# Optimization experiments

Measured on AMD Instinct MI355X. Metric: run time of the kernel, lower is better.

Reference implementation:

```python
import jax, jax.numpy as jnp
import numpy as np

N = 4096      # nodes
F = 128       # input feature dim
HEADS = 8     # attention_num
U = 8         # units per head


def setup_inputs() -> dict:
    key = jax.random.key(0)
    k_a, k_h, k_w, k_al, k_ar = jax.random.split(key, 5)
    A = jax.random.randint(k_a, (N, N), 0, 2).astype(jnp.float32)   # dense 0/1 adjacency
    H = jax.random.normal(k_h, (N, F), dtype=jnp.float32)
    W = jax.random.normal(k_w, (HEADS, F, U), dtype=jnp.float32) * 0.1
    a_left = jax.random.normal(k_al, (HEADS, U), dtype=jnp.float32) * 0.1
    a_right = jax.random.normal(k_ar, (HEADS, U), dtype=jnp.float32) * 0.1
    return {"A": A, "H": H, "W": W, "a_left": a_left, "a_right": a_right}


def reference(A, H, W, a_left, a_right):
    # Per-head attention logits: E[h,i,j] = e_left[h,i] + e_right[h,j]
    e_l = jnp.einsum('nf,hfu,hu->hn', H, W, a_left)    # [HEADS, N]
    e_r = jnp.einsum('nf,hfu,hu->hn', H, W, a_right)   # [HEADS, N]
    E = e_l[:, :, None] + e_r[:, None, :]              # [HEADS, N, N]
    # Faithful to original: denominator uses exp(E * A) (zeros in A -> exp(0)=1)
    denom = jnp.sum(jnp.exp(E * A[None]), axis=-1, keepdims=True)   # [HEADS, N, 1]
    Alpha = jnp.exp(E) / denom * A[None]               # masked attention weights
    # Aggregate then project: elu(Alpha @ H @ W) per head
    out = jax.nn.elu(jnp.einsum('hij,jf,hfu->hiu', Alpha, H, W))    # [HEADS, N, U]
    # is_output_layer=False -> concat heads along feature dim: [N, HEADS*U]
    return jnp.transpose(out, (1, 0, 2)).reshape(H.shape[0], HEADS * U)
```

## Files before the change

### kernel.cpp

```cpp
#include <hip/hip_runtime.h>
#include <hip/hip_bf16.h>

#define NN 4096
#define FF 128
#define NC 80
#define LSTR 84

typedef __attribute__((ext_vector_type(4))) float float4v;
typedef __attribute__((ext_vector_type(4))) unsigned int uint4v;
typedef __attribute__((ext_vector_type(8))) short short8;

static __device__ inline unsigned short bfb(float x) {
    __hip_bfloat16 b = __float2bfloat16(x);
    return *(unsigned short*)&b;
}
static __device__ inline float bff(unsigned short u) {
    __hip_bfloat16 b = *(__hip_bfloat16*)&u;
    return __bfloat162float(b);
}

__global__ __launch_bounds__(256) void gat_wsplit(const float* __restrict__ W,
                                                  const float* __restrict__ al,
                                                  const float* __restrict__ ar,
                                                  __hip_bfloat16* __restrict__ Wphi,
                                                  __hip_bfloat16* __restrict__ Wplo)
{
    const int tid = blockIdx.x * 256 + threadIdx.x;
    if (tid >= 80 * FF) return;
    const int c = tid % 80;
    const int f = tid / 80;
    float val;
    if (c < 64) {
        val = W[(size_t)(c >> 3) * (FF * 8) + (size_t)f * 8 + (c & 7)];
    } else {
        const int hc = (c - 64) & 7;
        const float* ap = (c < 72) ? ar : al;
        const float* wp = W + (size_t)hc * (FF * 8) + (size_t)f * 8;
        float s = 0.f;
        #pragma unroll
        for (int u = 0; u < 8; ++u) s += wp[u] * ap[hc * 8 + u];
        val = s;
    }
    const unsigned short h = bfb(val);
    const unsigned short l = bfb(val - bff(h));
    const int g = (f >> 5) * 4 + ((f >> 3) & 3);
    const size_t idx = ((size_t)g * NC + c) * 8 + (f & 7);
    Wphi[idx] = *(const __hip_bfloat16*)&h;
    Wplo[idx] = *(const __hip_bfloat16*)&l;
}

__global__ __launch_bounds__(64, 1) void gat_prep(const float* __restrict__ H,
                                                  const __hip_bfloat16* __restrict__ Wphi,
                                                  const __hip_bfloat16* __restrict__ Wplo,
                                                  float* __restrict__ expEl,
                                                  __hip_bfloat16* __restrict__ Bp)
{
    const int lane = threadIdx.x;
    const int j0 = blockIdx.x * 16;
    const int m16 = lane & 15, q = lane >> 4;
    const short* Whs = (const short*)Wphi;
    const short* Wls = (const short*)Wplo;

    float4v acc[5] = {};
    #pragma unroll
    for (int kt = 0; kt < 4; ++kt) {
        const float* hp = H + (size_t)(j0 + m16) * FF + kt * 32 + q * 8;
        float4v x0 = *(const float4v*)hp;
        float4v x1 = *(const float4v*)(hp + 4);
        short8 ahi, alo;
        #pragma unroll
        for (int i = 0; i < 4; ++i) {
            const unsigned short h0 = bfb(x0[i]);
            ahi[i] = (short)h0;
            alo[i] = (short)bfb(x0[i] - bff(h0));
            const unsigned short h1 = bfb(x1[i]);
            ahi[4 + i] = (short)h1;
            alo[4 + i] = (short)bfb(x1[i] - bff(h1));
        }
        const short8* bh = (const short8*)(Whs + (size_t)(kt * 4 + q) * NC * 8);
        const short8* bl = (const short8*)(Wls + (size_t)(kt * 4 + q) * NC * 8);
        #pragma unroll
        for (int nt = 0; nt < 5; ++nt) {
            short8 bhi = bh[nt * 16 + m16];
            short8 blo = bl[nt * 16 + m16];
            acc[nt] = __builtin_amdgcn_mfma_f32_16x16x32_bf16(ahi, bhi, acc[nt], 0, 0, 0);
            acc[nt] = __builtin_amdgcn_mfma_f32_16x16x32_bf16(alo, bhi, acc[nt], 0, 0, 0);
            acc[nt] = __builtin_amdgcn_mfma_f32_16x16x32_bf16(ahi, blo, acc[nt], 0, 0, 0);
        }
    }

    const int jbase = j0 + q * 4;
    float ex[4];
    #pragma unroll
    for (int r = 0; r < 4; ++r) ex[r] = expf(acc[4][r]);
    if (m16 >= 8) {
        #pragma unroll
        for (int r = 0; r < 4; ++r)
            expEl[(m16 - 8) * NN + jbase + r] = ex[r];
    }
    #pragma unroll
    for (int r = 0; r < 4; ++r) {
        const int j = jbase + r;
        const size_t base = ((size_t)((j >> 5) * 4 + ((j >> 3) & 3)) * NC) * 8 + (j & 7);
        #pragma unroll
        for (int nt = 0; nt < 4; ++nt) {
            const int srcl = (lane & 48) | (nt * 2 + (m16 >> 3));
            const float er = __shfl(ex[r], srcl);
            Bp[base + (size_t)(nt * 16 + m16) * 8] = __float2bfloat16(er * acc[nt][r]);
        }
        const float v = (m16 < 8) ? ex[r] : (m16 == 8 ? 1.0f : 0.0f);
        Bp[base + (size_t)(64 + m16) * 8] = __float2bfloat16(v);
    }
}

__global__ __launch_bounds__(512) void gat_gemm(const float* __restrict__ A,
                                                const __hip_bfloat16* __restrict__ Bp,
                                                const float* __restrict__ expEl,
                                                float* __restrict__ out)
{
    __shared__ float Ls[8 * 16 * LSTR];
    const int rb   = blockIdx.x;
    const int wave = threadIdx.x >> 6;
    const int lane = threadIdx.x & 63;
    const int m16  = lane & 15;
    const int q    = lane >> 4;
    const int row0 = rb * 16;

    float4v acc[5] = {};

    const int k0 = wave * 512;
    const unsigned int* Au = (const unsigned int*)A;
    const short* Bs = (const short*)Bp;
    const unsigned int* arow = Au + (size_t)(row0 + m16) * NN + q * 8;

    uint4v a0 = *(const uint4v*)(arow + k0);
    uint4v a1 = *(const uint4v*)(arow + k0 + 4);

    #pragma unroll 4
    for (int kt = 0; kt < 16; ++kt) {
        const int kk = k0 + kt * 32;
        short8 afrag;
        afrag[0] = (short)(a0[0] >> 16); afrag[1] = (short)(a0[1] >> 16);
        afrag[2] = (short)(a0[2] >> 16); afrag[3] = (short)(a0[3] >> 16);
        afrag[4] = (short)(a1[0] >> 16); afrag[5] = (short)(a1[1] >> 16);
        afrag[6] = (short)(a1[2] >> 16); afrag[7] = (short)(a1[3] >> 16);

        if (kt + 1 < 16) {
            a0 = *(const uint4v*)(arow + kk + 32);
            a1 = *(const uint4v*)(arow + kk + 36);
        }

        const int ktg = kk >> 5;
        const short8* bbase = (const short8*)(Bs + ((size_t)(ktg * 4 + q) * NC) * 8);
        #pragma unroll
        for (int nt = 0; nt < 5; ++nt) {
            short8 bfrag = bbase[nt * 16 + m16];
            acc[nt] = __builtin_amdgcn_mfma_f32_16x16x32_bf16(afrag, bfrag, acc[nt], 0, 0, 0);
        }
    }

    float* Lw = Ls + wave * (16 * LSTR);
    #pragma unroll
    for (int nt = 0; nt < 5; ++nt) {
        #pragma unroll
        for (int r = 0; r < 4; ++r)
            Lw[(q * 4 + r) * LSTR + nt * 16 + m16] = acc[nt][r];
    }
    __syncthreads();

    #pragma unroll
    for (int p = threadIdx.x; p < 1024; p += 512) {
        const int il = p >> 6;
        const int c  = p & 63;
        const int h  = c >> 3;
        float T = 0.f, S = 0.f, dg = 0.f;
        #pragma unroll
        for (int w = 0; w < 8; ++w) {
            const float* rowp = Ls + w * (16 * LSTR) + il * LSTR;
            T  += rowp[c];
            S  += rowp[64 + h];
            dg += rowp[72];
        }
        const float el = expEl[h * NN + row0 + il];
        const float denom = ((float)NN - dg) + el * S;
        const float x = el * T / denom;
        out[(size_t)(row0 + il) * 64 + c] = x > 0.f ? x : expf(x) - 1.f;
    }
}

extern "C" void kernel_launch(void* const* d_in, const int* in_sizes, int n_in,
                              void* d_out, int out_size, void* d_ws, size_t ws_size,
                              hipStream_t stream) {
    const float* A  = (const float*)d_in[0];
    const float* H  = (const float*)d_in[1];
    const float* W  = (const float*)d_in[2];
    const float* al = (const float*)d_in[3];
    const float* ar = (const float*)d_in[4];
    float* out = (float*)d_out;

    float* expEl = (float*)d_ws;
    __hip_bfloat16* Bp   = (__hip_bfloat16*)((char*)d_ws + 131072);
    __hip_bfloat16* Wphi = (__hip_bfloat16*)((char*)d_ws + 131072 + 655360);
    __hip_bfloat16* Wplo = (__hip_bfloat16*)((char*)d_ws + 131072 + 655360 + 20480);

    gat_wsplit<<<40, 256, 0, stream>>>(W, al, ar, Wphi, Wplo);
    gat_prep<<<NN / 16, 64, 0, stream>>>(H, Wphi, Wplo, expEl, Bp);
    gat_gemm<<<NN / 16, 512, 0, stream>>>(A, Bp, expEl, out);
}
```

Before: 119.8 us.

## Split prep K-loop across four waves and double-buffer A loads in GEMM

The prep kernel now runs four waves per block. Each wave handles one 32-wide K slice, the partial products are reduced through shared memory, and the exp/scaling and Bp/expEl writes are redistributed across 256 threads. This adds parallelism to a kernel that previously used a single wave per block. The GEMM kernel prefetches the A tiles two iterations ahead with a fully unrolled loop, to hide global load latency better. The cost is extra LDS traffic and a block barrier in prep, plus more registers in the GEMM.

```diff
diff --git a/kernel.cpp b/kernel.cpp
--- a/kernel.cpp
+++ b/kernel.cpp
@@ -49,67 +49,84 @@
     Wplo[idx] = *(const __hip_bfloat16*)&l;
 }
 
-__global__ __launch_bounds__(64, 1) void gat_prep(const float* __restrict__ H,
-                                                  const __hip_bfloat16* __restrict__ Wphi,
-                                                  const __hip_bfloat16* __restrict__ Wplo,
-                                                  float* __restrict__ expEl,
-                                                  __hip_bfloat16* __restrict__ Bp)
+__global__ __launch_bounds__(256) void gat_prep(const float* __restrict__ H,
+                                                const __hip_bfloat16* __restrict__ Wphi,
+                                                const __hip_bfloat16* __restrict__ Wplo,
+                                                float* __restrict__ expEl,
+                                                __hip_bfloat16* __restrict__ Bp)
 {
-    const int lane = threadIdx.x;
-    const int j0 = blockIdx.x * 16;
-    const int m16 = lane & 15, q = lane >> 4;
+    __shared__ float Lp[4 * 16 * LSTR];
+    const int t    = threadIdx.x;
+    const int wave = t >> 6;
+    const int lane = t & 63;
+    const int j0   = blockIdx.x * 16;
+    const int m16  = lane & 15, q = lane >> 4;
     const short* Whs = (const short*)Wphi;
     const short* Wls = (const short*)Wplo;
-
+    const int kt = wave;
+
+    const float* hp = H + (size_t)(j0 + m16) * FF + kt * 32 + q * 8;
+    float4v x0 = *(const float4v*)hp;
+    float4v x1 = *(const float4v*)(hp + 4);
+    short8 ahi, alo;
+    #pragma unroll
+    for (int i = 0; i < 4; ++i) {
+        const unsigned short h0 = bfb(x0[i]);
+        ahi[i] = (short)h0;
+        alo[i] = (short)bfb(x0[i] - bff(h0));
+        const unsigned short h1 = bfb(x1[i]);
+        ahi[4 + i] = (short)h1;
+        alo[4 + i] = (short)bfb(x1[i] - bff(h1));
+    }
+
+    const short8* bh = (const short8*)(Whs + (size_t)(kt * 4 + q) * NC * 8);
+    const short8* bl = (const short8*)(Wls + (size_t)(kt * 4 + q) * NC * 8);
     float4v acc[5] = {};
     #pragma unroll
-    for (int kt = 0; kt < 4; ++kt) {
-        const float* hp = H + (size_t)(j0 + m16) * FF + kt * 32 + q * 8;
-        float4v x0 = *(const float4v*)hp;
-        float4v x1 = *(const float4v*)(hp + 4);
-        short8 ahi, alo;
-        #pragma unroll
-        for (int i = 0; i < 4; ++i) {
-            const unsigned short h0 = bfb(x0[i]);
-            ahi[i] = (short)h0;
-            alo[i] = (short)bfb(x0[i] - bff(h0));
-            const unsigned short h1 = bfb(x1[i]);
-            ahi[4 + i] = (short)h1;
-            alo[4 + i] = (short)bfb(x1[i] - bff(h1));
-        }
-        const short8* bh = (const short8*)(Whs + (size_t)(kt * 4 + q) * NC * 8);
-        const short8* bl = (const short8*)(Wls + (size_t)(kt * 4 + q) * NC * 8);
-        #pragma unroll
-        for (int nt = 0; nt < 5; ++nt) {
-            short8 bhi = bh[nt * 16 + m16];
-            short8 blo = bl[nt * 16 + m16];
-            acc[nt] = __builtin_amdgcn_mfma_f32_16x16x32_bf16(ahi, bhi, acc[nt], 0, 0, 0);
-            acc[nt] = __builtin_amdgcn_mfma_f32_16x16x32_bf16(alo, bhi, acc[nt], 0, 0, 0);
-            acc[nt] = __builtin_amdgcn_mfma_f32_16x16x32_bf16(ahi, blo, acc[nt], 0, 0, 0);
-        }
-    }
-
-    const int jbase = j0 + q * 4;
-    float ex[4];
-    #pragma unroll
-    for (int r = 0; r < 4; ++r) ex[r] = expf(acc[4][r]);
-    if (m16 >= 8) {
+    for (int nt = 0; nt < 5; ++nt) {
+        short8 bhi = bh[nt * 16 + m16];
+        short8 blo = bl[nt * 16 + m16];
+        acc[nt] = __builtin_amdgcn_mfma_f32_16x16x32_bf16(ahi, bhi, acc[nt], 0, 0, 0);
+        acc[nt] = __builtin_amdgcn_mfma_f32_16x16x32_bf16(alo, bhi, acc[nt], 0, 0, 0);
+        acc[nt] = __builtin_amdgcn_mfma_f32_16x16x32_bf16(ahi, blo, acc[nt], 0, 0, 0);
+    }
+
+    float* Lw = Lp + wave * (16 * LSTR);
+    #pragma unroll
+    for (int nt = 0; nt < 5; ++nt) {
         #pragma unroll
         for (int r = 0; r < 4; ++r)
-            expEl[(m16 - 8) * NN + jbase + r] = ex[r];
-    }
-    #pragma unroll
-    for (int r = 0; r < 4; ++r) {
-        const int j = jbase + r;
-        const size_t base = ((size_t)((j >> 5) * 4 + ((j >> 3) & 3)) * NC) * 8 + (j & 7);
-        #pragma unroll
-        for (int nt = 0; nt < 4; ++nt) {
-            const int srcl = (lane & 48) | (nt * 2 + (m16 >> 3));
-            const float er = __shfl(ex[r], srcl);
-            Bp[base + (size_t)(nt * 16 + m16) * 8] = __float2bfloat16(er * acc[nt][r]);
-        }
-        const float v = (m16 < 8) ? ex[r] : (m16 == 8 ? 1.0f : 0.0f);
-        Bp[base + (size_t)(64 + m16) * 8] = __float2bfloat16(v);
+            Lw[(q * 4 + r) * LSTR + nt * 16 + m16] = acc[nt][r];
+    }
+    __syncthreads();
+
+    const int jl = t >> 4, g = t & 15;
+    const float* Lr = Lp + jl * LSTR;
+    const int jg = j0 + jl;
+    const size_t base = ((size_t)((jg >> 5) * 4 + ((jg >> 3) & 3)) * NC) * 8 + (jg & 7);
+
+    #pragma unroll
+    for (int i = 0; i < 4; ++i) {
+        const int c = g + 16 * i;
+        const int h = (g >> 3) + 2 * i;
+        const float er = expf(Lr[64 + h] + Lr[16 * LSTR + 64 + h] +
+                              Lr[32 * LSTR + 64 + h] + Lr[48 * LSTR + 64 + h]);
+        const float v = Lr[c] + Lr[16 * LSTR + c] +
+                        Lr[32 * LSTR + c] + Lr[48 * LSTR + c];
+        Bp[base + (size_t)c * 8] = __float2bfloat16(er * v);
+    }
+    float v64;
+    if (g < 8) {
+        v64 = expf(Lr[64 + g] + Lr[16 * LSTR + 64 + g] +
+                   Lr[32 * LSTR + 64 + g] + Lr[48 * LSTR + 64 + g]);
+    } else {
+        v64 = (g == 8) ? 1.0f : 0.0f;
+    }
+    Bp[base + (size_t)(64 + g) * 8] = __float2bfloat16(v64);
+    if (g >= 8) {
+        const int h = g - 8;
+        expEl[h * NN + jg] = expf(Lr[72 + h] + Lr[16 * LSTR + 72 + h] +
+                                  Lr[32 * LSTR + 72 + h] + Lr[48 * LSTR + 72 + h]);
     }
 }
 
@@ -131,26 +148,27 @@
     const int k0 = wave * 512;
     const unsigned int* Au = (const unsigned int*)A;
     const short* Bs = (const short*)Bp;
-    const unsigned int* arow = Au + (size_t)(row0 + m16) * NN + q * 8;
-
-    uint4v a0 = *(const uint4v*)(arow + k0);
-    uint4v a1 = *(const uint4v*)(arow + k0 + 4);
-
-    #pragma unroll 4
+    const unsigned int* arow = Au + (size_t)(row0 + m16) * NN + q * 8 + k0;
+
+    uint4v a0[2], a1[2];
+    a0[0] = *(const uint4v*)(arow);      a1[0] = *(const uint4v*)(arow + 4);
+    a0[1] = *(const uint4v*)(arow + 32); a1[1] = *(const uint4v*)(arow + 36);
+
+    #pragma unroll
     for (int kt = 0; kt < 16; ++kt) {
-        const int kk = k0 + kt * 32;
+        const int cur = kt & 1;
         short8 afrag;
-        afrag[0] = (short)(a0[0] >> 16); afrag[1] = (short)(a0[1] >> 16);
-        afrag[2] = (short)(a0[2] >> 16); afrag[3] = (short)(a0[3] >> 16);
-        afrag[4] = (short)(a1[0] >> 16); afrag[5] = (short)(a1[1] >> 16);
-        afrag[6] = (short)(a1[2] >> 16); afrag[7] = (short)(a1[3] >> 16);
-
-        if (kt + 1 < 16) {
-            a0 = *(const uint4v*)(arow + kk + 32);
-            a1 = *(const uint4v*)(arow + kk + 36);
+        afrag[0] = (short)(a0[cur][0] >> 16); afrag[1] = (short)(a0[cur][1] >> 16);
+        afrag[2] = (short)(a0[cur][2] >> 16); afrag[3] = (short)(a0[cur][3] >> 16);
+        afrag[4] = (short)(a1[cur][0] >> 16); afrag[5] = (short)(a1[cur][1] >> 16);
+        afrag[6] = (short)(a1[cur][2] >> 16); afrag[7] = (short)(a1[cur][3] >> 16);
+
+        if (kt + 2 < 16) {
+            a0[cur] = *(const uint4v*)(arow + (kt + 2) * 32);
+            a1[cur] = *(const uint4v*)(arow + (kt + 2) * 32 + 4);
         }
 
-        const int ktg = kk >> 5;
+        const int ktg = (k0 >> 5) + kt;
         const short8* bbase = (const short8*)(Bs + ((size_t)(ktg * 4 + q) * NC) * 8);
         #pragma unroll
         for (int nt = 0; nt < 5; ++nt) {
@@ -204,6 +222,6 @@
     __hip_bfloat16* Wplo = (__hip_bfloat16*)((char*)d_ws + 131072 + 655360 + 20480);
 
     gat_wsplit<<<40, 256, 0, stream>>>(W, al, ar, Wphi, Wplo);
-    gat_prep<<<NN / 16, 64, 0, stream>>>(H, Wphi, Wplo, expEl, Bp);
+    gat_prep<<<NN / 16, 256, 0, stream>>>(H, Wphi, Wplo, expEl, Bp);
     gat_gemm<<<NN / 16, 512, 0, stream>>>(A, Bp, expEl, out);
 }
```

After: 118.4 us. About the same (-1.1%).
